# Kernel optimization log

Measured on AMD Instinct MI355X. Metric: run time of the kernel, lower is better.

## Reference

```python
import jax, jax.numpy as jnp
import numpy as np

B, ACT, DICT = 4096, 768, 12288
TOP_K_AUX = 512
N_DEAD = 1024
AUX_PENALTY = 0.03125
SOFTMAX_AUX_PENALTY = 0.01
L1_COEFF = 0.001  # fraction=1 >= l1_warmup_frac -> full coeff
EPS = 1e-5


def setup_inputs() -> dict:
    key = jax.random.key(0)
    k1, k2, k3 = jax.random.split(key, 3)
    x = jax.random.normal(k1, (B, ACT), dtype=jnp.float32)
    # kaiming-uniform-scale init for W_enc, W_dec = normalized W_enc.T (as in __init__)
    bound = np.sqrt(6.0 / ACT)
    W_enc = jax.random.uniform(k2, (ACT, DICT), dtype=jnp.float32, minval=-bound, maxval=bound)
    W_dec = W_enc.T
    W_dec = W_dec / jnp.linalg.norm(W_dec, axis=-1, keepdims=True)
    b_enc = jnp.zeros((DICT,), dtype=jnp.float32)
    b_dec = jnp.zeros((ACT,), dtype=jnp.float32)
    quantile_threshold = jnp.full((1,), 0.1, dtype=jnp.float32)
    dead_features = jnp.zeros((DICT,), dtype=bool).at[:N_DEAD].set(True)
    return {"x": x, "W_enc": W_enc, "W_dec": W_dec, "b_enc": b_enc,
            "b_dec": b_dec, "quantile_threshold": quantile_threshold,
            "dead_features": dead_features}


def reference(x, W_enc, W_dec, b_enc, b_dec, quantile_threshold, dead_features):
    # input unit-norm (torch .std uses ddof=1)
    x_mean = jnp.mean(x, axis=-1, keepdims=True)
    x = x - x_mean
    x_std = jnp.std(x, axis=-1, keepdims=True, ddof=1)
    x = x / (x_std + EPS)

    x_cent = x - b_dec
    acts_pre = x_cent @ W_enc + b_enc          # [B, DICT]
    acts = jax.nn.relu(acts_pre)

    acts_mask = acts > quantile_threshold
    acts_thresholded = acts * acts_mask
    x_reconstruct = acts_thresholded @ W_dec + b_dec  # [B, ACT]

    residual = x - x_reconstruct

    # aux path 1: topk over dead features only (dead count >= TOP_K_AUX by setup)
    neg_inf = jnp.asarray(-jnp.inf, dtype=acts.dtype)
    masked_acts = jnp.where(dead_features, acts, neg_inf)
    vals, idx = jax.lax.top_k(masked_acts, TOP_K_AUX)  # [B, K]
    rows = jnp.arange(B)[:, None]
    acts_aux = jnp.zeros_like(acts).at[rows, idx].set(vals)  # nonzero only on dead cols
    x_reconstruct_aux = acts_aux @ W_dec + b_dec
    l2_loss_aux = AUX_PENALTY * jnp.mean((x_reconstruct_aux - residual) ** 2)

    # aux path 2: softmax-weighted pre-activations over dead features
    acts_softmax_aux = acts_pre * jax.nn.softmax(acts_pre, axis=-1) * 64.0
    x_reconstruct_softmax = (acts_softmax_aux * dead_features) @ W_dec + b_dec
    l2_loss_softmax = SOFTMAX_AUX_PENALTY * jnp.mean((x_reconstruct_softmax - residual) ** 2)

    l2_loss = jnp.mean((x_reconstruct - x) ** 2)
    l1_norm = jnp.mean(jnp.sum(jnp.abs(acts_thresholded), axis=-1))
    l1_loss = L1_COEFF * l1_norm
    l0_norm = jnp.mean(jnp.sum((acts_thresholded > 0).astype(jnp.float32), axis=-1))

    loss = l2_loss + l1_loss + l2_loss_aux + l2_loss_softmax

    # final rescale (as written in source: * x_std + x, with x the normalized input)
    sae_out = x_reconstruct * x_std + x
    num_dead = jnp.sum(dead_features.astype(jnp.int32))
    return (sae_out, acts_thresholded, loss, l2_loss, l1_loss, l0_norm,
            l1_norm, l2_loss_aux, l2_loss_softmax, num_dead)
```

## Files before the change

kernel.cpp:

```cpp
#include <hip/hip_runtime.h>

#define B_    4096
#define ACT   768
#define DICT  12288
#define KTOP  512
#define NDMAX 1024
#define AUX_PEN  0.03125f
#define SOFT_PEN 0.01f
#define L1_CO    0.001f
#define EPS_     1e-5f
#define NBLK_FE  1536
#define PLANE    (B_ * ACT)
#define SPLITK2  4
#define SPLITK3  2

typedef __attribute__((ext_vector_type(4))) float f32x4;
typedef __attribute__((ext_vector_type(4))) unsigned int u32x4;
typedef __attribute__((ext_vector_type(8))) short short8;
typedef __attribute__((ext_vector_type(8))) __bf16 bf8_t;

__device__ __forceinline__ float b2f(unsigned short u) {
    return __uint_as_float(((unsigned)u) << 16);
}
__device__ __forceinline__ unsigned short f2b(float f) {
    unsigned u = __float_as_uint(f);
    unsigned r = (u + 0x7FFFu + ((u >> 16) & 1u)) >> 16;
    return (unsigned short)r;
}

__device__ __forceinline__ float wredsum(float v) {
#pragma unroll
    for (int o = 32; o; o >>= 1) v += __shfl_down(v, o);
    return v;
}
__device__ __forceinline__ float wredmax(float v) {
#pragma unroll
    for (int o = 32; o; o >>= 1) v = fmaxf(v, __shfl_down(v, o));
    return v;
}
__device__ __forceinline__ int wredsumi(int v) {
#pragma unroll
    for (int o = 32; o; o >>= 1) v += __shfl_down(v, o);
    return v;
}
__device__ __forceinline__ float bredsum(float v, float* sh) {
    int lane = threadIdx.x & 63, w = threadIdx.x >> 6;
    v = wredsum(v);
    __syncthreads();
    if (!lane) sh[w] = v;
    __syncthreads();
    return sh[0] + sh[1] + sh[2] + sh[3];
}
__device__ __forceinline__ float bredmax(float v, float* sh) {
    int lane = threadIdx.x & 63, w = threadIdx.x >> 6;
    v = wredmax(v);
    __syncthreads();
    if (!lane) sh[w] = v;
    __syncthreads();
    return fmaxf(fmaxf(sh[0], sh[1]), fmaxf(sh[2], sh[3]));
}
__device__ __forceinline__ int bredsumi(int v, int* sh) {
    int lane = threadIdx.x & 63, w = threadIdx.x >> 6;
    v = wredsumi(v);
    __syncthreads();
    if (!lane) sh[w] = v;
    __syncthreads();
    return sh[0] + sh[1] + sh[2] + sh[3];
}

__device__ __forceinline__ void gload16(const void* g, const void* lds_base) {
    __builtin_amdgcn_global_load_lds((const __attribute__((address_space(1))) void*)g,
                                     (__attribute__((address_space(3))) void*)lds_base,
                                     16, 0, 0);
}

__global__ __launch_bounds__(256) void norm_kernel(
    const float* __restrict__ x, float* __restrict__ xn,
    unsigned short* __restrict__ xnb, float* __restrict__ xstd)
{
    __shared__ float sh[4];
    const int row = blockIdx.x, t = threadIdx.x;
    const float* xr = x + (size_t)row * ACT;
    float v0 = xr[t], v1 = xr[t + 256], v2 = xr[t + 512];
    float s = bredsum(v0 + v1 + v2, sh);
    float mean = s * (1.0f / ACT);
    v0 -= mean; v1 -= mean; v2 -= mean;
    float s2 = bredsum(v0 * v0 + v1 * v1 + v2 * v2, sh);
    float sd = sqrtf(s2 / (float)(ACT - 1));
    float inv = 1.0f / (sd + EPS_);
    v0 *= inv; v1 *= inv; v2 *= inv;
    size_t base = (size_t)row * ACT;
    xn[base + t] = v0; xn[base + t + 256] = v1; xn[base + t + 512] = v2;
    xnb[base + t] = f2b(v0); xnb[base + t + 256] = f2b(v1); xnb[base + t + 512] = f2b(v2);
    if (!t) xstd[row] = sd;
}

__global__ __launch_bounds__(256) void transpose_bf16(
    const float* __restrict__ in, unsigned short* __restrict__ out, int R, int C)
{
    __shared__ float tile[64][65];
    const int c0 = blockIdx.x * 64, r0 = blockIdx.y * 64;
    const int t = threadIdx.x;
#pragma unroll
    for (int i = 0; i < 16; i++) {
        int lin = t + i * 256;
        int r = lin >> 6, c = lin & 63;
        tile[r][c] = in[(size_t)(r0 + r) * C + c0 + c];
    }
    __syncthreads();
#pragma unroll
    for (int i = 0; i < 16; i++) {
        int lin = t + i * 256;
        int cc = lin >> 6, rr = lin & 63;
        out[(size_t)(c0 + cc) * R + r0 + rr] = f2b(tile[rr][cc]);
    }
}

__global__ __launch_bounds__(256) void cvec_kernel(
    const float* __restrict__ benc, const float* __restrict__ bdec,
    const float* __restrict__ wenc, float* __restrict__ cvec)
{
    int j = blockIdx.x * 256 + threadIdx.x;
    float acc = 0.f;
    for (int k = 0; k < ACT; k++) acc += bdec[k] * wenc[(size_t)k * DICT + j];
    cvec[j] = benc[j] - acc;
}

__global__ __launch_bounds__(256) void dead_scan(
    const void* __restrict__ dead_raw, int* __restrict__ dead_list, int* __restrict__ ndp)
{
    __shared__ int cnt[256];
    const unsigned char* u8 = (const unsigned char*)dead_raw;
    const unsigned* u32p = (const unsigned*)dead_raw;
    unsigned w0 = u32p[0];
    int mode;
    if (w0 == 0x01010101u) mode = 1;
    else if (w0 == 0x3F800000u) mode = 2;
    else if (w0 == 1u) mode = 0;
    else mode = (u8[1] | u8[2] | u8[3]) ? 1 : 0;

    const int t = threadIdx.x;
    const int per = DICT / 256;
    const int base = t * per;
    int c = 0;
    for (int i = 0; i < per; i++) {
        int j = base + i;
        bool d = (mode == 1) ? (u8[j] != 0)
               : (mode == 2) ? (((const float*)dead_raw)[j] != 0.f)
                             : (((const int*)dead_raw)[j] != 0);
        c += d ? 1 : 0;
    }
    cnt[t] = c;
    __syncthreads();
    if (!t) {
        int run = 0;
        for (int i = 0; i < 256; i++) { int v = cnt[i]; cnt[i] = run; run += v; }
        *ndp = run;
    }
    __syncthreads();
    int o = cnt[t];
    for (int i = 0; i < per; i++) {
        int j = base + i;
        bool d = (mode == 1) ? (u8[j] != 0)
               : (mode == 2) ? (((const float*)dead_raw)[j] != 0.f)
                             : (((const int*)dead_raw)[j] != 0);
        if (d) dead_list[o++] = j;
    }
}

__global__ __launch_bounds__(256) void gemm1_kernel(
    const unsigned short* __restrict__ A, const unsigned short* __restrict__ Bt,
    const float* __restrict__ cvec, unsigned short* __restrict__ actspre)
{
    __shared__ __align__(16) unsigned short As[2][128 * 32];
    __shared__ __align__(16) unsigned short Bs[2][128 * 32];
    const int tid = threadIdx.x, lane = tid & 63, wave = tid >> 6;
    const int wr = wave >> 1, wc = wave & 1;
    const int lr = lane & 15, lg = lane >> 4;
    const int flat = blockIdx.x;
    const int xcd = flat & 7, j = flat >> 3;
    const int col0 = (xcd * 12 + (j >> 5)) * 128;
    const int row0 = (j & 31) * 128;
    const int nsteps = ACT / 32;
    f32x4 acc[4][4] = {};

    auto stage = [&](int kt, int b) {
#pragma unroll
        for (int i = 0; i < 2; i++) {
            int c = wave * 2 + i;
            int o = c * 1024;
            int ol = o + lane * 16;
            int r = ol >> 6;
            int cb = (ol & 63) ^ (((r >> 1) & 3) << 4);
            gload16((const char*)A + (size_t)(row0 + r) * (ACT * 2) + kt * 2 + cb,
                    (const char*)As[b] + o);
            gload16((const char*)Bt + (size_t)(col0 + r) * (ACT * 2) + kt * 2 + cb,
                    (const char*)Bs[b] + o);
        }
    };

    stage(0, 0);
    __syncthreads();
    int cur = 0;
    for (int t = 0; t < nsteps; ++t) {
        const int nxt = cur ^ 1;
        if (t + 1 < nsteps) stage((t + 1) * 32, nxt);
        bf8_t af[4], bfr[4];
#pragma unroll
        for (int m = 0; m < 4; m++) {
            int row = wr * 64 + m * 16 + lr;
            af[m] = *(const bf8_t*)((const char*)As[cur] + row * 64 + ((lg * 16) ^ (((row >> 1) & 3) << 4)));
        }
#pragma unroll
        for (int n = 0; n < 4; n++) {
            int col = wc * 64 + n * 16 + lr;
            bfr[n] = *(const bf8_t*)((const char*)Bs[cur] + col * 64 + ((lg * 16) ^ (((col >> 1) & 3) << 4)));
        }
#pragma unroll
        for (int m = 0; m < 4; m++)
#pragma unroll
            for (int n = 0; n < 4; n++)
                acc[m][n] = __builtin_amdgcn_mfma_f32_16x16x32_bf16(af[m], bfr[n], acc[m][n], 0, 0, 0);
        __syncthreads();
        cur = nxt;
    }
#pragma unroll
    for (int m = 0; m < 4; m++) {
        int row = row0 + wr * 64 + m * 16 + lg * 4;
#pragma unroll
        for (int n = 0; n < 4; n++) {
            int col = col0 + wc * 64 + n * 16 + lr;
            float cadd = cvec[col];
#pragma unroll
            for (int r = 0; r < 4; r++) {
                float v = acc[m][n][r] + cadd;
                actspre[(size_t)(row + r) * DICT + col] = f2b(v);
            }
        }
    }
}

__global__ __launch_bounds__(256) void softrow_kernel(
    unsigned short* __restrict__ actspre, const float* __restrict__ qtp,
    const int* __restrict__ dead_list, const int* __restrict__ ndp,
    unsigned short* __restrict__ asoft, unsigned short* __restrict__ aaux,
    float* __restrict__ l1row, float* __restrict__ l0row,
    float* __restrict__ out_thr)
{
    __shared__ __align__(16) unsigned short rowv[DICT];
    __shared__ float shf[4];
    __shared__ int shi[4];
    const int t = threadIdx.x, row = blockIdx.x;
    unsigned short* src = actspre + (size_t)row * DICT;
    float* othr = out_thr + (size_t)row * DICT;
    short8 v[6];
    float mx = -1e30f;
#pragma unroll
    for (int i = 0; i < 6; i++) {
        v[i] = *(const short8*)(src + i * 2048 + t * 8);
        *(short8*)(rowv + i * 2048 + t * 8) = v[i];
#pragma unroll
        for (int e = 0; e < 8; e++) mx = fmaxf(mx, b2f((unsigned short)v[i][e]));
    }
    mx = bredmax(mx, shf);
    const float qt = fmaxf(qtp[0], 0.0f);
    float se = 0.f, l1 = 0.f, l0 = 0.f;
#pragma unroll
    for (int i = 0; i < 6; i++) {
        short8 tvv;
        float tvf[8];
#pragma unroll
        for (int e = 0; e < 8; e++) {
            float f = b2f((unsigned short)v[i][e]);
            se += __expf(f - mx);
            float a = fmaxf(f, 0.f);
            float tv = (a > qt) ? a : 0.f;
            l1 += tv;
            l0 += (tv > 0.f) ? 1.f : 0.f;
            tvv[e] = (tv > 0.f) ? v[i][e] : (short)0;
            tvf[e] = tv;
        }
        *(short8*)(src + i * 2048 + t * 8) = tvv;
        float* od = othr + i * 2048 + t * 8;
        *(f32x4*)od       = (f32x4){ tvf[0], tvf[1], tvf[2], tvf[3] };
        *(f32x4*)(od + 4) = (f32x4){ tvf[4], tvf[5], tvf[6], tvf[7] };
    }
    se = bredsum(se, shf);
    l1 = bredsum(l1, shf);
    l0 = bredsum(l0, shf);
    if (!t) { l1row[row] = l1; l0row[row] = l0; }

    float inv64 = 64.0f / se;
    int nd = *ndp; if (nd > NDMAX) nd = NDMAX;
    unsigned k16[4]; float av_[4];
#pragma unroll
    for (int i = 0; i < 4; i++) {
        int k = t + i * 256;
        float f = 0.f;
        if (k < nd) {
            int idx = dead_list[k];
            f = b2f(rowv[idx]);
            asoft[(size_t)row * NDMAX + k] = f2b(f * __expf(f - mx) * inv64);
        } else {
            asoft[(size_t)row * NDMAX + k] = 0;
        }
        float a = (k < nd) ? fmaxf(f, 0.f) : 0.f;
        av_[i] = a;
        k16[i] = __float_as_uint(a) >> 16;
    }
    unsigned lo = 0u, hi = 0x7F80u;
    while (hi - lo > 1u) {
        unsigned mid = (lo + hi) >> 1;
        int c = 0;
#pragma unroll
        for (int i = 0; i < 4; i++) c += (k16[i] >= mid) ? 1 : 0;
        c = bredsumi(c, shi);
        if (c >= KTOP) lo = mid; else hi = mid;
    }
#pragma unroll
    for (int i = 0; i < 4; i++) {
        int k = t + i * 256;
        aaux[(size_t)row * NDMAX + k] = f2b((k16[i] >= lo) ? av_[i] : 0.f);
    }
}

__global__ __launch_bounds__(256) void wdead_gather(
    const unsigned short* __restrict__ wdec_t, const int* __restrict__ dead_list,
    const int* __restrict__ ndp, unsigned short* __restrict__ wdead)
{
    int n = blockIdx.x;
    int nd = *ndp; if (nd > NDMAX) nd = NDMAX;
    for (int k = threadIdx.x; k < NDMAX; k += 256)
        wdead[(size_t)n * NDMAX + k] = (k < nd) ? wdec_t[(size_t)n * DICT + dead_list[k]] : 0;
}

__global__ __launch_bounds__(256) void gemm2_kernel(
    const unsigned short* __restrict__ Apre, const unsigned short* __restrict__ Bt,
    float* __restrict__ pxrA, float* __restrict__ pxrB)
{
    __shared__ __align__(16) unsigned short As[2][128 * 32];
    __shared__ __align__(16) unsigned short Bs[2][128 * 32];
    const int tid = threadIdx.x, lane = tid & 63, wave = tid >> 6;
    const int wr = wave >> 1, wc = wave & 1;
    const int lr = lane & 15, lg = lane >> 4;
    const int flat = blockIdx.x;
    const int xcd = flat & 7, s = flat >> 3;
    const int q = s / 6, m_ = s - 6 * q;
    const int g = q * 8 + xcd;
    const int col0 = m_ * 128;
    const int row0 = (g & 31) * 128;
    const int zidx = g >> 5;
    const int kbase = zidx * (DICT / SPLITK2);
    const int nsteps = (DICT / SPLITK2) / 32;
    f32x4 acc[4][4] = {};

    auto stage = [&](int kt, int b) {
#pragma unroll
        for (int i = 0; i < 2; i++) {
            int c = wave * 2 + i;
            int o = c * 1024;
            int ol = o + lane * 16;
            int r = ol >> 6;
            int cb = (ol & 63) ^ (((r >> 1) & 3) << 4);
            gload16((const char*)Apre + (size_t)(row0 + r) * (DICT * 2) + (size_t)kt * 2 + cb,
                    (const char*)As[b] + o);
            gload16((const char*)Bt + (size_t)(col0 + r) * (DICT * 2) + (size_t)kt * 2 + cb,
                    (const char*)Bs[b] + o);
        }
    };

    stage(kbase, 0);
    __syncthreads();
    int cur = 0;
    for (int t = 0; t < nsteps; ++t) {
        const int nxt = cur ^ 1;
        if (t + 1 < nsteps) stage(kbase + (t + 1) * 32, nxt);
        bf8_t af[4], bfr[4];
#pragma unroll
        for (int m = 0; m < 4; m++) {
            int row = wr * 64 + m * 16 + lr;
            af[m] = *(const bf8_t*)((const char*)As[cur] + row * 64 + ((lg * 16) ^ (((row >> 1) & 3) << 4)));
        }
#pragma unroll
        for (int n = 0; n < 4; n++) {
            int col = wc * 64 + n * 16 + lr;
            bfr[n] = *(const bf8_t*)((const char*)Bs[cur] + col * 64 + ((lg * 16) ^ (((col >> 1) & 3) << 4)));
        }
#pragma unroll
        for (int m = 0; m < 4; m++)
#pragma unroll
            for (int n = 0; n < 4; n++)
                acc[m][n] = __builtin_amdgcn_mfma_f32_16x16x32_bf16(af[m], bfr[n], acc[m][n], 0, 0, 0);
        __syncthreads();
        cur = nxt;
    }
    float* out = (zidx < 2) ? (pxrA + (size_t)zidx * PLANE)
                            : (pxrB + (size_t)(zidx - 2) * PLANE);
#pragma unroll
    for (int m = 0; m < 4; m++) {
        int row = row0 + wr * 64 + m * 16 + lg * 4;
#pragma unroll
        for (int n = 0; n < 4; n++) {
            int col = col0 + wc * 64 + n * 16 + lr;
#pragma unroll
            for (int r = 0; r < 4; r++)
                out[(size_t)(row + r) * ACT + col] = acc[m][n][r];
        }
    }
}

__global__ __launch_bounds__(256) void gemm3_kernel(
    const unsigned short* __restrict__ A1, const unsigned short* __restrict__ A2,
    const unsigned short* __restrict__ Bt,
    float* __restrict__ praux, float* __restrict__ prsoft)
{
    __shared__ __align__(16) unsigned short A1s[128 * 64];
    __shared__ __align__(16) unsigned short A2s[128 * 64];
    __shared__ __align__(16) unsigned short Bs[128 * 64];
    const int tid = threadIdx.x, lane = tid & 63, wave = tid >> 6;
    const int wr = wave >> 1, wc = wave & 1;
    const int lr = lane & 15, lg = lane >> 4;
    const int flat = blockIdx.x;
    const int xcd = flat & 7, s = flat >> 3;
    const int q = s / 6, m_ = s - 6 * q;
    const int g = q * 8 + xcd;
    const int col0 = m_ * 128;
    const int row0 = (g & 31) * 128;
    const int zidx = g >> 5;
    const int kbase = zidx * (NDMAX / SPLITK3);
    const int kend  = kbase + (NDMAX / SPLITK3);
    f32x4 acc1[4][4] = {}, acc2[4][4] = {};

    for (int kt = kbase; kt < kend; kt += 64) {
#pragma unroll
        for (int i = 0; i < 4; i++) {
            int chunk = wave * 4 + i;
            int o = chunk * 1024;
            int ol = o + lane * 16;
            int r = ol >> 7;
            int b = (ol & 127) ^ ((r & 7) << 4);
            gload16((const char*)A1 + (size_t)(row0 + r) * (NDMAX * 2) + kt * 2 + b, (const char*)A1s + o);
            gload16((const char*)A2 + (size_t)(row0 + r) * (NDMAX * 2) + kt * 2 + b, (const char*)A2s + o);
            gload16((const char*)Bt + (size_t)(col0 + r) * (NDMAX * 2) + kt * 2 + b, (const char*)Bs + o);
        }
        __syncthreads();
#pragma unroll
        for (int kk = 0; kk < 64; kk += 32) {
            bf8_t a1f[4], a2f[4], bfr[4];
#pragma unroll
            for (int m = 0; m < 4; m++) {
                int row = wr * 64 + m * 16 + lr;
                int bo = (kk * 2 + lg * 16) ^ ((row & 7) << 4);
                a1f[m] = *(const bf8_t*)((const char*)A1s + row * 128 + bo);
                a2f[m] = *(const bf8_t*)((const char*)A2s + row * 128 + bo);
            }
#pragma unroll
            for (int n = 0; n < 4; n++) {
                int col = wc * 64 + n * 16 + lr;
                bfr[n] = *(const bf8_t*)((const char*)Bs + col * 128 + ((kk * 2 + lg * 16) ^ ((col & 7) << 4)));
            }
#pragma unroll
            for (int m = 0; m < 4; m++)
#pragma unroll
                for (int n = 0; n < 4; n++) {
                    acc1[m][n] = __builtin_amdgcn_mfma_f32_16x16x32_bf16(a1f[m], bfr[n], acc1[m][n], 0, 0, 0);
                    acc2[m][n] = __builtin_amdgcn_mfma_f32_16x16x32_bf16(a2f[m], bfr[n], acc2[m][n], 0, 0, 0);
                }
        }
        __syncthreads();
    }
    float* o1 = praux  + (size_t)zidx * PLANE;
    float* o2 = prsoft + (size_t)zidx * PLANE;
#pragma unroll
    for (int m = 0; m < 4; m++) {
        int row = row0 + wr * 64 + m * 16 + lg * 4;
#pragma unroll
        for (int n = 0; n < 4; n++) {
            int col = col0 + wc * 64 + n * 16 + lr;
#pragma unroll
            for (int r = 0; r < 4; r++) {
                size_t idx = (size_t)(row + r) * ACT + col;
                o1[idx] = acc1[m][n][r];
                o2[idx] = acc2[m][n][r];
            }
        }
    }
}

__global__ __launch_bounds__(256) void final_elem(
    const float* __restrict__ pxrA, const float* __restrict__ pxrB,
    const float* __restrict__ praux, const float* __restrict__ prsoft,
    const float* __restrict__ xn, const float* __restrict__ xstd,
    const float* __restrict__ bdec,
    float* __restrict__ sae_out, float* __restrict__ partials)
{
    __shared__ float sh[4];
    const int t = threadIdx.x, blk = blockIdx.x;
    const int base = blk * 2048;
    float s2 = 0.f, sa = 0.f, ss = 0.f;
#pragma unroll
    for (int i = 0; i < 8; i++) {
        int idx = base + t + i * 256;
        int row = idx / ACT;
        int col = idx - row * ACT;
        float bd = bdec[col];
        float r  = pxrA[idx] + pxrA[PLANE + idx] + pxrB[idx] + pxrB[PLANE + idx] + bd;
        float ra = praux[idx] + praux[PLANE + idx] + bd;
        float rs = prsoft[idx] + prsoft[PLANE + idx] + bd;
        float xv = xn[idx];
        float resid = xv - r;
        float da = ra - resid;
        float dsf = rs - resid;
        s2 += resid * resid;
        sa += da * da;
        ss += dsf * dsf;
        sae_out[idx] = r * xstd[row] + xv;
    }
    s2 = bredsum(s2, sh);
    sa = bredsum(sa, sh);
    ss = bredsum(ss, sh);
    if (!t) {
        partials[blk] = s2;
        partials[NBLK_FE + blk] = sa;
        partials[2 * NBLK_FE + blk] = ss;
    }
}

__global__ __launch_bounds__(256) void final_scalar(
    const float* __restrict__ partials, const float* __restrict__ l1row,
    const float* __restrict__ l0row, const int* __restrict__ ndp,
    float* __restrict__ out_sc)
{
    __shared__ float sh[4];
    const int t = threadIdx.x;
    float s2 = 0.f, sa = 0.f, ss = 0.f;
    for (int i = t; i < NBLK_FE; i += 256) {
        s2 += partials[i];
        sa += partials[NBLK_FE + i];
        ss += partials[2 * NBLK_FE + i];
    }
    s2 = bredsum(s2, sh);
    sa = bredsum(sa, sh);
    ss = bredsum(ss, sh);
    float l1 = 0.f, l0 = 0.f;
    for (int i = t; i < B_; i += 256) { l1 += l1row[i]; l0 += l0row[i]; }
    l1 = bredsum(l1, sh);
    l0 = bredsum(l0, sh);
    if (!t) {
        const float n = (float)B_ * (float)ACT;
        float l2   = s2 / n;
        float l2a  = AUX_PEN  * (sa / n);
        float l2s  = SOFT_PEN * (ss / n);
        float l1n  = l1 / (float)B_;
        float l1l  = L1_CO * l1n;
        float l0n  = l0 / (float)B_;
        float loss = l2 + l1l + l2a + l2s;
        out_sc[0] = loss;
        out_sc[1] = l2;
        out_sc[2] = l1l;
        out_sc[3] = l0n;
        out_sc[4] = l1n;
        out_sc[5] = l2a;
        out_sc[6] = l2s;
        out_sc[7] = (float)(*ndp);
    }
}

extern "C" void kernel_launch(void* const* d_in, const int* in_sizes, int n_in,
                              void* d_out, int out_size, void* d_ws, size_t ws_size,
                              hipStream_t stream)
{
    const float* x    = (const float*)d_in[0];
    const float* Wenc = (const float*)d_in[1];
    const float* Wdec = (const float*)d_in[2];
    const float* benc = (const float*)d_in[3];
    const float* bdec = (const float*)d_in[4];
    const float* qtp  = (const float*)d_in[5];
    const void*  dead = d_in[6];

    float* out_sae = (float*)d_out;
    float* out_thr = out_sae + (size_t)B_ * ACT;
    float* out_sc  = out_thr + (size_t)B_ * DICT;

    char* w = (char*)d_ws;
    auto alloc = [&](size_t bytes) -> char* {
        char* p = w;
        w += (bytes + 255) & ~(size_t)255;
        return p;
    };
    float*          xn      = (float*)alloc((size_t)B_ * ACT * 4);
    unsigned short* xnb     = (unsigned short*)alloc((size_t)B_ * ACT * 2);
    unsigned short* wenc_t  = (unsigned short*)alloc((size_t)DICT * ACT * 2);
    unsigned short* wdec_t  = (unsigned short*)alloc((size_t)ACT * DICT * 2);
    float*          cvec    = (float*)alloc((size_t)DICT * 4);
    unsigned short* actspre = (unsigned short*)alloc((size_t)B_ * DICT * 2);
    unsigned short* asoft   = (unsigned short*)alloc((size_t)B_ * NDMAX * 2);
    unsigned short* aaux    = (unsigned short*)alloc((size_t)B_ * NDMAX * 2);
    unsigned short* wdead   = (unsigned short*)alloc((size_t)ACT * NDMAX * 2);
    float*          xstd    = (float*)alloc((size_t)B_ * 4);
    float*          l1row   = (float*)alloc((size_t)B_ * 4);
    float*          l0row   = (float*)alloc((size_t)B_ * 4);
    float*          partials= (float*)alloc((size_t)3 * NBLK_FE * 4);
    int*            dlist   = (int*)alloc((size_t)DICT * 4);
    int*            ndp     = (int*)alloc(256);
    float*          pxrB    = (float*)alloc((size_t)2 * PLANE * 4);

    float* pxrA = (float*)xnb;
    float* praux  = (float*)actspre;
    float* prsoft = praux + (size_t)SPLITK3 * PLANE;

    norm_kernel<<<B_, 256, 0, stream>>>(x, xn, xnb, xstd);
    transpose_bf16<<<dim3(DICT / 64, ACT / 64), 256, 0, stream>>>(Wenc, wenc_t, ACT, DICT);
    transpose_bf16<<<dim3(ACT / 64, DICT / 64), 256, 0, stream>>>(Wdec, wdec_t, DICT, ACT);
    cvec_kernel<<<DICT / 256, 256, 0, stream>>>(benc, bdec, Wenc, cvec);
    dead_scan<<<1, 256, 0, stream>>>(dead, dlist, ndp);
    gemm1_kernel<<<3072, 256, 0, stream>>>(xnb, wenc_t, cvec, actspre);
    softrow_kernel<<<B_, 256, 0, stream>>>(actspre, qtp, dlist, ndp, asoft, aaux, l1row, l0row, out_thr);
    wdead_gather<<<ACT, 256, 0, stream>>>(wdec_t, dlist, ndp, wdead);
    gemm2_kernel<<<768, 256, 0, stream>>>(actspre, wdec_t, pxrA, pxrB);
    gemm3_kernel<<<384, 256, 0, stream>>>(aaux, asoft, wdead, praux, prsoft);
    final_elem<<<NBLK_FE, 256, 0, stream>>>(pxrA, pxrB, praux, prsoft, xn, xstd, bdec, out_sae, partials);
    final_scalar<<<1, 256, 0, stream>>>(partials, l1row, l0row, ndp, out_sc);
}
```

Before: 494.7 us.

## Merge decoder and aux GEMMs into one launch with separate aux buffer

```diff
diff --git a/kernel.cpp b/kernel.cpp
--- a/kernel.cpp
+++ b/kernel.cpp
@@ -334,17 +334,15 @@
         wdead[(size_t)n * NDMAX + k] = (k < nd) ? wdec_t[(size_t)n * DICT + dead_list[k]] : 0;
 }
 
-__global__ __launch_bounds__(256) void gemm2_kernel(
+__device__ __forceinline__ void gemm2_body(
+    char* lds, int flatblk,
     const unsigned short* __restrict__ Apre, const unsigned short* __restrict__ Bt,
     float* __restrict__ pxrA, float* __restrict__ pxrB)
 {
-    __shared__ __align__(16) unsigned short As[2][128 * 32];
-    __shared__ __align__(16) unsigned short Bs[2][128 * 32];
     const int tid = threadIdx.x, lane = tid & 63, wave = tid >> 6;
     const int wr = wave >> 1, wc = wave & 1;
     const int lr = lane & 15, lg = lane >> 4;
-    const int flat = blockIdx.x;
-    const int xcd = flat & 7, s = flat >> 3;
+    const int xcd = flatblk & 7, s = flatblk >> 3;
     const int q = s / 6, m_ = s - 6 * q;
     const int g = q * 8 + xcd;
     const int col0 = m_ * 128;
@@ -353,7 +351,6 @@
     const int kbase = zidx * (DICT / SPLITK2);
     const int nsteps = (DICT / SPLITK2) / 32;
     f32x4 acc[4][4] = {};
-
     auto stage = [&](int kt, int b) {
 #pragma unroll
         for (int i = 0; i < 2; i++) {
@@ -363,9 +360,9 @@
             int r = ol >> 6;
             int cb = (ol & 63) ^ (((r >> 1) & 3) << 4);
             gload16((const char*)Apre + (size_t)(row0 + r) * (DICT * 2) + (size_t)kt * 2 + cb,
-                    (const char*)As[b] + o);
+                    lds + b * 8192 + o);
             gload16((const char*)Bt + (size_t)(col0 + r) * (DICT * 2) + (size_t)kt * 2 + cb,
-                    (const char*)Bs[b] + o);
+                    lds + 16384 + b * 8192 + o);
         }
     };
 
@@ -379,12 +376,12 @@
 #pragma unroll
         for (int m = 0; m < 4; m++) {
             int row = wr * 64 + m * 16 + lr;
-            af[m] = *(const bf8_t*)((const char*)As[cur] + row * 64 + ((lg * 16) ^ (((row >> 1) & 3) << 4)));
+            af[m] = *(const bf8_t*)(lds + cur * 8192 + row * 64 + ((lg * 16) ^ (((row >> 1) & 3) << 4)));
         }
 #pragma unroll
         for (int n = 0; n < 4; n++) {
             int col = wc * 64 + n * 16 + lr;
-            bfr[n] = *(const bf8_t*)((const char*)Bs[cur] + col * 64 + ((lg * 16) ^ (((col >> 1) & 3) << 4)));
+            bfr[n] = *(const bf8_t*)(lds + 16384 + cur * 8192 + col * 64 + ((lg * 16) ^ (((col >> 1) & 3) << 4)));
         }
 #pragma unroll
         for (int m = 0; m < 4; m++)
@@ -409,19 +406,16 @@
     }
 }
 
-__global__ __launch_bounds__(256) void gemm3_kernel(
+__device__ __forceinline__ void gemm3_body(
+    char* lds, int flatblk,
     const unsigned short* __restrict__ A1, const unsigned short* __restrict__ A2,
     const unsigned short* __restrict__ Bt,
     float* __restrict__ praux, float* __restrict__ prsoft)
 {
-    __shared__ __align__(16) unsigned short A1s[128 * 64];
-    __shared__ __align__(16) unsigned short A2s[128 * 64];
-    __shared__ __align__(16) unsigned short Bs[128 * 64];
     const int tid = threadIdx.x, lane = tid & 63, wave = tid >> 6;
     const int wr = wave >> 1, wc = wave & 1;
     const int lr = lane & 15, lg = lane >> 4;
-    const int flat = blockIdx.x;
-    const int xcd = flat & 7, s = flat >> 3;
+    const int xcd = flatblk & 7, s = flatblk >> 3;
     const int q = s / 6, m_ = s - 6 * q;
     const int g = q * 8 + xcd;
     const int col0 = m_ * 128;
@@ -430,7 +424,6 @@
     const int kbase = zidx * (NDMAX / SPLITK3);
     const int kend  = kbase + (NDMAX / SPLITK3);
     f32x4 acc1[4][4] = {}, acc2[4][4] = {};
-
     for (int kt = kbase; kt < kend; kt += 64) {
 #pragma unroll
         for (int i = 0; i < 4; i++) {
@@ -439,9 +432,9 @@
             int ol = o + lane * 16;
             int r = ol >> 7;
             int b = (ol & 127) ^ ((r & 7) << 4);
-            gload16((const char*)A1 + (size_t)(row0 + r) * (NDMAX * 2) + kt * 2 + b, (const char*)A1s + o);
-            gload16((const char*)A2 + (size_t)(row0 + r) * (NDMAX * 2) + kt * 2 + b, (const char*)A2s + o);
-            gload16((const char*)Bt + (size_t)(col0 + r) * (NDMAX * 2) + kt * 2 + b, (const char*)Bs + o);
+            gload16((const char*)A1 + (size_t)(row0 + r) * (NDMAX * 2) + kt * 2 + b, lds + o);
+            gload16((const char*)A2 + (size_t)(row0 + r) * (NDMAX * 2) + kt * 2 + b, lds + 16384 + o);
+            gload16((const char*)Bt + (size_t)(col0 + r) * (NDMAX * 2) + kt * 2 + b, lds + 32768 + o);
         }
         __syncthreads();
 #pragma unroll
@@ -451,13 +444,13 @@
             for (int m = 0; m < 4; m++) {
                 int row = wr * 64 + m * 16 + lr;
                 int bo = (kk * 2 + lg * 16) ^ ((row & 7) << 4);
-                a1f[m] = *(const bf8_t*)((const char*)A1s + row * 128 + bo);
-                a2f[m] = *(const bf8_t*)((const char*)A2s + row * 128 + bo);
+                a1f[m] = *(const bf8_t*)(lds + row * 128 + bo);
+                a2f[m] = *(const bf8_t*)(lds + 16384 + row * 128 + bo);
             }
 #pragma unroll
             for (int n = 0; n < 4; n++) {
                 int col = wc * 64 + n * 16 + lr;
-                bfr[n] = *(const bf8_t*)((const char*)Bs + col * 128 + ((kk * 2 + lg * 16) ^ ((col & 7) << 4)));
+                bfr[n] = *(const bf8_t*)(lds + 32768 + col * 128 + ((kk * 2 + lg * 16) ^ ((col & 7) << 4)));
             }
 #pragma unroll
             for (int m = 0; m < 4; m++)
@@ -484,6 +477,38 @@
                 o2[idx] = acc2[m][n][r];
             }
         }
+    }
+}
+
+__global__ __launch_bounds__(256) void gemm2_kernel(
+    const unsigned short* __restrict__ Apre, const unsigned short* __restrict__ Bt,
+    float* __restrict__ pxrA, float* __restrict__ pxrB)
+{
+    __shared__ __align__(16) char lds[32768];
+    gemm2_body(lds, blockIdx.x, Apre, Bt, pxrA, pxrB);
+}
+
+__global__ __launch_bounds__(256) void gemm3_kernel(
+    const unsigned short* __restrict__ A1, const unsigned short* __restrict__ A2,
+    const unsigned short* __restrict__ Bt,
+    float* __restrict__ praux, float* __restrict__ prsoft)
+{
+    __shared__ __align__(16) char lds[49152];
+    gemm3_body(lds, blockIdx.x, A1, A2, Bt, praux, prsoft);
+}
+
+__global__ __launch_bounds__(256) void gemm23_kernel(
+    const unsigned short* __restrict__ Apre, const unsigned short* __restrict__ BtDec,
+    float* __restrict__ pxrA, float* __restrict__ pxrB,
+    const unsigned short* __restrict__ A1, const unsigned short* __restrict__ A2,
+    const unsigned short* __restrict__ BtDead,
+    float* __restrict__ praux, float* __restrict__ prsoft)
+{
+    __shared__ __align__(16) char lds[49152];
+    if (blockIdx.x < 768) {
+        gemm2_body(lds, blockIdx.x, Apre, BtDec, pxrA, pxrB);
+    } else {
+        gemm3_body(lds, blockIdx.x - 768, A1, A2, BtDead, praux, prsoft);
     }
 }
 
@@ -606,7 +631,10 @@
     float*          pxrB    = (float*)alloc((size_t)2 * PLANE * 4);
 
     float* pxrA = (float*)xnb;
-    float* praux  = (float*)actspre;
+
+    float* prauxM = (float*)alloc((size_t)4 * PLANE * 4);
+    const bool merged = ((size_t)(w - (char*)d_ws) <= ws_size);
+    float* praux  = merged ? prauxM : (float*)actspre;
     float* prsoft = praux + (size_t)SPLITK3 * PLANE;
 
     norm_kernel<<<B_, 256, 0, stream>>>(x, xn, xnb, xstd);
@@ -617,8 +645,13 @@
     gemm1_kernel<<<3072, 256, 0, stream>>>(xnb, wenc_t, cvec, actspre);
     softrow_kernel<<<B_, 256, 0, stream>>>(actspre, qtp, dlist, ndp, asoft, aaux, l1row, l0row, out_thr);
     wdead_gather<<<ACT, 256, 0, stream>>>(wdec_t, dlist, ndp, wdead);
-    gemm2_kernel<<<768, 256, 0, stream>>>(actspre, wdec_t, pxrA, pxrB);
-    gemm3_kernel<<<384, 256, 0, stream>>>(aaux, asoft, wdead, praux, prsoft);
+    if (merged) {
+        gemm23_kernel<<<768 + 384, 256, 0, stream>>>(actspre, wdec_t, pxrA, pxrB,
+                                                     aaux, asoft, wdead, praux, prsoft);
+    } else {
+        gemm2_kernel<<<768, 256, 0, stream>>>(actspre, wdec_t, pxrA, pxrB);
+        gemm3_kernel<<<384, 256, 0, stream>>>(aaux, asoft, wdead, praux, prsoft);
+    }
     final_elem<<<NBLK_FE, 256, 0, stream>>>(pxrA, pxrB, praux, prsoft, xn, xstd, bdec, out_sae, partials);
     final_scalar<<<1, 256, 0, stream>>>(partials, l1row, l0row, ndp, out_sc);
 }
```

Result: slower. 553.0 us (+11.8%).
